# Kernel tuning notes

Measured on AMD Instinct MI355X. Metric: run time of the kernel, lower is better.

Reference implementation:

```python
import jax, jax.numpy as jnp
from jax import lax
import numpy as np

WINDOW_SIZE = 11
SIGMA = 1.5
C1 = 0.01 ** 2
C2 = 0.03 ** 2


def _make_window(window_size, channel):
    x = np.arange(window_size) - window_size // 2
    g = np.exp(-(x ** 2) / (2.0 * SIGMA ** 2))
    g = g / g.sum()
    w3 = g[:, None, None] * g[None, :, None] * g[None, None, :]  # [k,k,k]
    w = np.broadcast_to(w3, (channel, 1, window_size, window_size, window_size))
    return jnp.asarray(w.copy(), dtype=jnp.float32)


def setup_inputs() -> dict:
    key = jax.random.key(0)
    k1, k2 = jax.random.split(key)
    shape = (4, 1, 160, 160, 160)
    img1 = jax.random.uniform(k1, shape, dtype=jnp.float32)
    img2 = jax.random.uniform(k2, shape, dtype=jnp.float32)
    window = _make_window(WINDOW_SIZE, shape[1])
    return {"img1": img1, "img2": img2, "window": window}


def _depthwise_conv3d(x, window):
    c = window.shape[0]
    k = window.shape[-1]
    pad = k // 2
    return lax.conv_general_dilated(
        x, window,
        window_strides=(1, 1, 1),
        padding=[(pad, pad)] * 3,
        dimension_numbers=("NCDHW", "OIDHW", "NCDHW"),
        feature_group_count=c,
    )


def reference(img1, img2, window):
    b = img1.shape[0]
    # One conv call over all five window statistics (stacked along batch).
    stacked = jnp.concatenate(
        [img1, img2, img1 * img1, img2 * img2, img1 * img2], axis=0)
    conv = _depthwise_conv3d(stacked, window)
    mu1, mu2, e11, e22, e12 = (conv[i * b:(i + 1) * b] for i in range(5))
    mu1_sq = mu1 * mu1
    mu2_sq = mu2 * mu2
    mu1_mu2 = mu1 * mu2
    sigma1_sq = e11 - mu1_sq
    sigma2_sq = e22 - mu2_sq
    sigma12 = e12 - mu1_mu2
    ssim_map = ((2 * mu1_mu2 + C1) * (2 * sigma12 + C2)) / (
        (mu1_sq + mu2_sq + C1) * (sigma1_sq + sigma2_sq + C2))
    return ssim_map.mean()  # size_average=True
```

## Files before the change

### kernel.cpp

```cpp
#include <hip/hip_runtime.h>
#include <math.h>

typedef float f2 __attribute__((ext_vector_type(2)));
typedef float f4 __attribute__((ext_vector_type(4)));

#define DD 160
#define HH 160
#define WW 160
#define BB 4
#define KK 11
#define RAD 5
#define TH 16
#define TW 16
#define DCH 32
#define NPLANES (DCH + 2 * RAD)
#define NDCH (DD / DCH)
#define HALO_H (TH + 2 * RAD)
#define TS 16

struct GaussW { float g[KK]; };

__global__ __launch_bounds__(128, 3)
void ssim3d_kernel(const float* __restrict__ img1,
                   const float* __restrict__ img2,
                   float* __restrict__ out, GaussW gw)
{
    __shared__ float tmp[2][5][HALO_H * TS];
    __shared__ float wsum[2];

    const int tid = threadIdx.x;
    const int xc = tid & 7;
    const int ty = tid >> 3;
    const int p1r = tid >> 2;
    const int p1q = tid & 3;

    const int blk = blockIdx.x;
    const int bw = blk % 10;
    const int bh = (blk / 10) % 10;
    const int bd = (blk / 100) % NDCH;
    const int bb = blk / (100 * NDCH);

    const int oh0 = bh * TH, ow0 = bw * TW, od0 = bd * DCH;
    const float* base1 = img1 + (size_t)bb * DD * HH * WW;
    const float* base2 = img2 + (size_t)bb * DD * HH * WW;

    float g[KK];
#pragma unroll
    for (int i = 0; i < KK; ++i) g[i] = gw.g[i];

    f2 a1[KK], a2[KK], a11[KK], a22[KK], a12[KK];
#pragma unroll
    for (int i = 0; i < KK; ++i) { a1[i]=0.f; a2[i]=0.f; a11[i]=0.f; a22[i]=0.f; a12[i]=0.f; }

    f2 lsum = 0.f;

    const int gh = oh0 - RAD + p1r;
    const bool p1act = (p1r < HALO_H);
    const bool rowok = p1act && ((unsigned)gh < (unsigned)HH);
    const int gc0 = ow0 + 4 * p1q - 8;
    const size_t rowoff = (size_t)((unsigned)gh < (unsigned)HH ? gh : 0) * WW;

    for (int p = 0; p < NPLANES; ++p) {
        const int d = od0 - RAD + p;
        const bool dval = ((unsigned)d < (unsigned)DD);
        const int buf = p & 1;

        if (dval) {
            if (p1act) {
                float t1[4]  = {0.f,0.f,0.f,0.f};
                float t2[4]  = {0.f,0.f,0.f,0.f};
                float t11[4] = {0.f,0.f,0.f,0.f};
                float t22[4] = {0.f,0.f,0.f,0.f};
                float t12[4] = {0.f,0.f,0.f,0.f};
                const size_t pb = (size_t)d * HH * WW + rowoff;
#pragma unroll
                for (int j = 0; j < 5; ++j) {
                    const int gc = gc0 + 4 * j;
                    f4 av4 = {0.f,0.f,0.f,0.f};
                    f4 bv4 = {0.f,0.f,0.f,0.f};
                    if (rowok && gc >= 0 && gc <= WW - 4) {
                        av4 = *(const f4*)(base1 + pb + gc);
                        bv4 = *(const f4*)(base2 + pb + gc);
                    }
#pragma unroll
                    for (int ii = 0; ii < 4; ++ii) {
                        const int i = 4 * j + ii;
                        if (i < 3 || i > 16) continue;
                        const float av = av4[ii], bv = bv4[ii];
                        const float aa = av * av, bb2 = bv * bv, ab = av * bv;
#pragma unroll
                        for (int m = 0; m < 4; ++m) {
                            const int k = i - m - 3;
                            if (k >= 0 && k < KK) {
                                const float w = g[k];
                                t1[m]  += w * av;
                                t2[m]  += w * bv;
                                t11[m] += w * aa;
                                t22[m] += w * bb2;
                                t12[m] += w * ab;
                            }
                        }
                    }
                }
                const int tb = p1r * TS + 4 * p1q;
                f4 v;
                v[0]=t1[0];  v[1]=t1[1];  v[2]=t1[2];  v[3]=t1[3];  *(f4*)&tmp[buf][0][tb] = v;
                v[0]=t2[0];  v[1]=t2[1];  v[2]=t2[2];  v[3]=t2[3];  *(f4*)&tmp[buf][1][tb] = v;
                v[0]=t11[0]; v[1]=t11[1]; v[2]=t11[2]; v[3]=t11[3]; *(f4*)&tmp[buf][2][tb] = v;
                v[0]=t22[0]; v[1]=t22[1]; v[2]=t22[2]; v[3]=t22[3]; *(f4*)&tmp[buf][3][tb] = v;
                v[0]=t12[0]; v[1]=t12[1]; v[2]=t12[2]; v[3]=t12[3]; *(f4*)&tmp[buf][4][tb] = v;
            }
            __syncthreads();

            f2 P1 = 0.f, P2 = 0.f, P11 = 0.f, P22 = 0.f, P12 = 0.f;
#pragma unroll
            for (int k = 0; k < KK; ++k) {
                const float w = g[k];
                const int off = (ty + k) * TS + 2 * xc;
                f2 v;
                v = *(const f2*)&tmp[buf][0][off]; P1  += w * v;
                v = *(const f2*)&tmp[buf][1][off]; P2  += w * v;
                v = *(const f2*)&tmp[buf][2][off]; P11 += w * v;
                v = *(const f2*)&tmp[buf][3][off]; P22 += w * v;
                v = *(const f2*)&tmp[buf][4][off]; P12 += w * v;
            }
#pragma unroll
            for (int i = 0; i < KK; ++i) {
                const float w = g[KK - 1 - i];
                a1[i]  += w * P1;
                a2[i]  += w * P2;
                a11[i] += w * P11;
                a22[i] += w * P22;
                a12[i] += w * P12;
            }
        }

        if (p >= 2 * RAD) {
            f2 mu1 = a1[0], mu2 = a2[0];
            f2 m11 = mu1 * mu1, m22 = mu2 * mu2, m12 = mu1 * mu2;
            f2 sg1 = a11[0] - m11, sg2 = a22[0] - m22, sg12 = a12[0] - m12;
            const float C1c = 0.0001f, C2c = 0.0009f;
            f2 num = (2.f * m12 + C1c) * (2.f * sg12 + C2c);
            f2 den = (m11 + m22 + C1c) * (sg1 + sg2 + C2c);
            lsum += num / den;
        }
#pragma unroll
        for (int i = 0; i < KK - 1; ++i) {
            a1[i] = a1[i+1]; a2[i] = a2[i+1]; a11[i] = a11[i+1];
            a22[i] = a22[i+1]; a12[i] = a12[i+1];
        }
        a1[KK-1]=0.f; a2[KK-1]=0.f; a11[KK-1]=0.f; a22[KK-1]=0.f; a12[KK-1]=0.f;
    }

    float v = lsum.x + lsum.y;
#pragma unroll
    for (int off = 32; off > 0; off >>= 1)
        v += __shfl_down(v, off, 64);
    if ((tid & 63) == 0) wsum[tid >> 6] = v;
    __syncthreads();
    if (tid == 0) {
        const float inv_n = 1.0f / ((float)BB * DD * HH * WW);
        atomicAdd(out, (wsum[0] + wsum[1]) * inv_n);
    }
}

extern "C" void kernel_launch(void* const* d_in, const int* in_sizes, int n_in,
                              void* d_out, int out_size, void* d_ws, size_t ws_size,
                              hipStream_t stream) {
    const float* img1 = (const float*)d_in[0];
    const float* img2 = (const float*)d_in[1];
    float* out = (float*)d_out;

    GaussW gw;
    double gd[KK], sum = 0.0;
    for (int i = 0; i < KK; ++i) {
        double x = (double)(i - KK / 2);
        gd[i] = exp(-(x * x) / (2.0 * 1.5 * 1.5));
        sum += gd[i];
    }
    for (int i = 0; i < KK; ++i) gw.g[i] = (float)(gd[i] / sum);

    hipMemsetAsync(d_out, 0, sizeof(float), stream);

    dim3 grid(10 * 10 * NDCH * BB);
    dim3 block(128);
    hipLaunchKernelGGL(ssim3d_kernel, grid, block, 0, stream,
                       img1, img2, out, gw);
}
```

Baseline: 343.9 us.

## Prefetch next depth plane into registers and rotate depth accumulators by unrolling

Global loads for the next depth plane are issued into registers before the current plane's LDS pass, so memory latency can overlap compute. The depth loop is unrolled by 11 with compile-time ring indices, which removes the per-plane shift of 55 accumulator registers. The launch-bounds occupancy hint drops from 3 to 2 to make room for the extra registers. This trades fewer resident waves for more latency hiding, and the 44-iteration loop with p < NPLANES guards runs two wasted iterations.

New measurement: 335.0 us. -2.6%, faster.

```diff
diff --git a/kernel.cpp b/kernel.cpp
--- a/kernel.cpp
+++ b/kernel.cpp
@@ -1,5 +1,6 @@
 #include <hip/hip_runtime.h>
 #include <math.h>
+#include <type_traits>
 
 typedef float f2 __attribute__((ext_vector_type(2)));
 typedef float f4 __attribute__((ext_vector_type(4)));
@@ -17,15 +18,17 @@
 #define NDCH (DD / DCH)
 #define HALO_H (TH + 2 * RAD)
 #define TS 16
+#define STAT (HALO_H * TS)
 
 struct GaussW { float g[KK]; };
 
-__global__ __launch_bounds__(128, 3)
+__global__ __launch_bounds__(128, 2)
 void ssim3d_kernel(const float* __restrict__ img1,
                    const float* __restrict__ img2,
                    float* __restrict__ out, GaussW gw)
 {
-    __shared__ float tmp[2][5][HALO_H * TS];
+    __shared__ float tmpA[5 * STAT];
+    __shared__ float tmpB[5 * STAT];
     __shared__ float wsum[2];
 
     const int tid = threadIdx.x;
@@ -60,96 +63,146 @@
     const int gc0 = ow0 + 4 * p1q - 8;
     const size_t rowoff = (size_t)((unsigned)gh < (unsigned)HH ? gh : 0) * WW;
 
-    for (int p = 0; p < NPLANES; ++p) {
+    f4 pa[5], pb[5];
+#pragma unroll
+    for (int j = 0; j < 5; ++j) { pa[j] = (f4)0.f; pb[j] = (f4)0.f; }
+
+    float* twr = tmpA;
+    float* trd = tmpB;
+
+    {
+        const int dn = od0 - RAD;
+        if (p1act && (unsigned)dn < (unsigned)DD) {
+            const size_t pbv = (size_t)dn * (HH * WW) + rowoff;
+#pragma unroll
+            for (int j = 0; j < 5; ++j) {
+                const int gc = gc0 + 4 * j;
+                f4 za = (f4)0.f, zb = (f4)0.f;
+                if (rowok && gc >= 0 && gc <= WW - 4) {
+                    za = *(const f4*)(base1 + pbv + gc);
+                    zb = *(const f4*)(base2 + pbv + gc);
+                }
+                pa[j] = za; pb[j] = zb;
+            }
+        }
+    }
+
+    int pcbase = 0;
+    auto body = [&](auto uc) {
+        constexpr int U = decltype(uc)::value;
+        const int p = pcbase + U;
         const int d = od0 - RAD + p;
-        const bool dval = ((unsigned)d < (unsigned)DD);
-        const int buf = p & 1;
-
-        if (dval) {
-            if (p1act) {
-                float t1[4]  = {0.f,0.f,0.f,0.f};
-                float t2[4]  = {0.f,0.f,0.f,0.f};
-                float t11[4] = {0.f,0.f,0.f,0.f};
-                float t22[4] = {0.f,0.f,0.f,0.f};
-                float t12[4] = {0.f,0.f,0.f,0.f};
-                const size_t pb = (size_t)d * HH * WW + rowoff;
-#pragma unroll
-                for (int j = 0; j < 5; ++j) {
-                    const int gc = gc0 + 4 * j;
-                    f4 av4 = {0.f,0.f,0.f,0.f};
-                    f4 bv4 = {0.f,0.f,0.f,0.f};
-                    if (rowok && gc >= 0 && gc <= WW - 4) {
-                        av4 = *(const f4*)(base1 + pb + gc);
-                        bv4 = *(const f4*)(base2 + pb + gc);
-                    }
-#pragma unroll
-                    for (int ii = 0; ii < 4; ++ii) {
-                        const int i = 4 * j + ii;
-                        if (i < 3 || i > 16) continue;
-                        const float av = av4[ii], bv = bv4[ii];
-                        const float aa = av * av, bb2 = bv * bv, ab = av * bv;
-#pragma unroll
-                        for (int m = 0; m < 4; ++m) {
-                            const int k = i - m - 3;
-                            if (k >= 0 && k < KK) {
-                                const float w = g[k];
-                                t1[m]  += w * av;
-                                t2[m]  += w * bv;
-                                t11[m] += w * aa;
-                                t22[m] += w * bb2;
-                                t12[m] += w * ab;
-                            }
+        const bool dval = (p < NPLANES) && ((unsigned)d < (unsigned)DD);
+
+        if (dval && p1act) {
+            float t1[4]  = {0.f,0.f,0.f,0.f};
+            float t2[4]  = {0.f,0.f,0.f,0.f};
+            float t11[4] = {0.f,0.f,0.f,0.f};
+            float t22[4] = {0.f,0.f,0.f,0.f};
+            float t12[4] = {0.f,0.f,0.f,0.f};
+#pragma unroll
+            for (int j = 0; j < 5; ++j) {
+#pragma unroll
+                for (int ii = 0; ii < 4; ++ii) {
+                    const int i = 4 * j + ii;
+                    if (i < 3 || i > 16) continue;
+                    const float av = pa[j][ii], bv = pb[j][ii];
+                    const float aa = av * av, bb2 = bv * bv, ab = av * bv;
+#pragma unroll
+                    for (int m = 0; m < 4; ++m) {
+                        const int k = i - m - 3;
+                        if (k >= 0 && k < KK) {
+                            const float w = g[k];
+                            t1[m]  += w * av;
+                            t2[m]  += w * bv;
+                            t11[m] += w * aa;
+                            t22[m] += w * bb2;
+                            t12[m] += w * ab;
                         }
                     }
                 }
-                const int tb = p1r * TS + 4 * p1q;
-                f4 v;
-                v[0]=t1[0];  v[1]=t1[1];  v[2]=t1[2];  v[3]=t1[3];  *(f4*)&tmp[buf][0][tb] = v;
-                v[0]=t2[0];  v[1]=t2[1];  v[2]=t2[2];  v[3]=t2[3];  *(f4*)&tmp[buf][1][tb] = v;
-                v[0]=t11[0]; v[1]=t11[1]; v[2]=t11[2]; v[3]=t11[3]; *(f4*)&tmp[buf][2][tb] = v;
-                v[0]=t22[0]; v[1]=t22[1]; v[2]=t22[2]; v[3]=t22[3]; *(f4*)&tmp[buf][3][tb] = v;
-                v[0]=t12[0]; v[1]=t12[1]; v[2]=t12[2]; v[3]=t12[3]; *(f4*)&tmp[buf][4][tb] = v;
-            }
+            }
+            float* tw = twr + p1r * TS + 4 * p1q;
+            f4 v;
+            v[0]=t1[0];  v[1]=t1[1];  v[2]=t1[2];  v[3]=t1[3];  *(f4*)(tw + 0*STAT) = v;
+            v[0]=t2[0];  v[1]=t2[1];  v[2]=t2[2];  v[3]=t2[3];  *(f4*)(tw + 1*STAT) = v;
+            v[0]=t11[0]; v[1]=t11[1]; v[2]=t11[2]; v[3]=t11[3]; *(f4*)(tw + 2*STAT) = v;
+            v[0]=t22[0]; v[1]=t22[1]; v[2]=t22[2]; v[3]=t22[3]; *(f4*)(tw + 3*STAT) = v;
+            v[0]=t12[0]; v[1]=t12[1]; v[2]=t12[2]; v[3]=t12[3]; *(f4*)(tw + 4*STAT) = v;
+        }
+
+        {
+            const int pn = p + 1;
+            const int dn = od0 - RAD + pn;
+            if (p1act && (pn < NPLANES) && ((unsigned)dn < (unsigned)DD)) {
+                const size_t pbv = (size_t)dn * (HH * WW) + rowoff;
+#pragma unroll
+                for (int j = 0; j < 5; ++j) {
+                    const int gc = gc0 + 4 * j;
+                    f4 za = (f4)0.f, zb = (f4)0.f;
+                    if (rowok && gc >= 0 && gc <= WW - 4) {
+                        za = *(const f4*)(base1 + pbv + gc);
+                        zb = *(const f4*)(base2 + pbv + gc);
+                    }
+                    pa[j] = za; pb[j] = zb;
+                }
+            }
+        }
+
+        if (dval) {
             __syncthreads();
-
             f2 P1 = 0.f, P2 = 0.f, P11 = 0.f, P22 = 0.f, P12 = 0.f;
+            const float* tb = twr + (ty * TS + 2 * xc);
 #pragma unroll
             for (int k = 0; k < KK; ++k) {
                 const float w = g[k];
-                const int off = (ty + k) * TS + 2 * xc;
-                f2 v;
-                v = *(const f2*)&tmp[buf][0][off]; P1  += w * v;
-                v = *(const f2*)&tmp[buf][1][off]; P2  += w * v;
-                v = *(const f2*)&tmp[buf][2][off]; P11 += w * v;
-                v = *(const f2*)&tmp[buf][3][off]; P22 += w * v;
-                v = *(const f2*)&tmp[buf][4][off]; P12 += w * v;
-            }
-#pragma unroll
-            for (int i = 0; i < KK; ++i) {
-                const float w = g[KK - 1 - i];
-                a1[i]  += w * P1;
-                a2[i]  += w * P2;
-                a11[i] += w * P11;
-                a22[i] += w * P22;
-                a12[i] += w * P12;
-            }
-        }
-
-        if (p >= 2 * RAD) {
-            f2 mu1 = a1[0], mu2 = a2[0];
+                const int o = k * TS;
+                P1  += w * *(const f2*)(tb + 0*STAT + o);
+                P2  += w * *(const f2*)(tb + 1*STAT + o);
+                P11 += w * *(const f2*)(tb + 2*STAT + o);
+                P22 += w * *(const f2*)(tb + 3*STAT + o);
+                P12 += w * *(const f2*)(tb + 4*STAT + o);
+            }
+#pragma unroll
+            for (int t = 0; t < KK; ++t) {
+                constexpr int base = U + 22;
+                const int s = (base - t) % 11;
+                const float w = g[t];
+                a1[s]  += w * P1;
+                a2[s]  += w * P2;
+                a11[s] += w * P11;
+                a22[s] += w * P22;
+                a12[s] += w * P12;
+            }
+        }
+
+        constexpr int e = (U + 1) % 11;
+        if (p >= 2 * RAD && p < NPLANES) {
+            f2 mu1 = a1[e], mu2 = a2[e];
             f2 m11 = mu1 * mu1, m22 = mu2 * mu2, m12 = mu1 * mu2;
-            f2 sg1 = a11[0] - m11, sg2 = a22[0] - m22, sg12 = a12[0] - m12;
+            f2 sg1 = a11[e] - m11, sg2 = a22[e] - m22, sg12 = a12[e] - m12;
             const float C1c = 0.0001f, C2c = 0.0009f;
             f2 num = (2.f * m12 + C1c) * (2.f * sg12 + C2c);
             f2 den = (m11 + m22 + C1c) * (sg1 + sg2 + C2c);
             lsum += num / den;
         }
-#pragma unroll
-        for (int i = 0; i < KK - 1; ++i) {
-            a1[i] = a1[i+1]; a2[i] = a2[i+1]; a11[i] = a11[i+1];
-            a22[i] = a22[i+1]; a12[i] = a12[i+1];
-        }
-        a1[KK-1]=0.f; a2[KK-1]=0.f; a11[KK-1]=0.f; a22[KK-1]=0.f; a12[KK-1]=0.f;
+        a1[e] = 0.f; a2[e] = 0.f; a11[e] = 0.f; a22[e] = 0.f; a12[e] = 0.f;
+
+        float* t = twr; twr = trd; trd = t;
+    };
+
+    for (pcbase = 0; pcbase < 44; pcbase += 11) {
+        body(std::integral_constant<int, 0>{});
+        body(std::integral_constant<int, 1>{});
+        body(std::integral_constant<int, 2>{});
+        body(std::integral_constant<int, 3>{});
+        body(std::integral_constant<int, 4>{});
+        body(std::integral_constant<int, 5>{});
+        body(std::integral_constant<int, 6>{});
+        body(std::integral_constant<int, 7>{});
+        body(std::integral_constant<int, 8>{});
+        body(std::integral_constant<int, 9>{});
+        body(std::integral_constant<int, 10>{});
     }
 
     float v = lsum.x + lsum.y;
```
